# Performance work log

Hardware: AMD Instinct MI355X
Metric: run time of the kernel (lower is better)

Reference implementation:

```python
import jax, jax.numpy as jnp
from jax import lax
import numpy as np

B, T, IN, H, NC = 2048, 512, 1, 128, 8


def setup_inputs() -> dict:
    key = jax.random.key(0)
    ks = jax.random.split(key, 13)
    s = 0.05
    inp = {
        "x": jax.random.normal(ks[0], (B, T, IN), dtype=jnp.float32),
        # layer 0 LSTM params (PyTorch layout: W_ih [4H, in], W_hh [4H, H])
        "W_ih0": jax.random.normal(ks[1], (4 * H, IN), dtype=jnp.float32) * s,
        "W_hh0": jax.random.normal(ks[2], (4 * H, H), dtype=jnp.float32) * s,
        "b_ih0": jax.random.normal(ks[3], (4 * H,), dtype=jnp.float32) * s,
        "b_hh0": jax.random.normal(ks[4], (4 * H,), dtype=jnp.float32) * s,
        # layer 1 LSTM params
        "W_ih1": jax.random.normal(ks[5], (4 * H, H), dtype=jnp.float32) * s,
        "W_hh1": jax.random.normal(ks[6], (4 * H, H), dtype=jnp.float32) * s,
        "b_ih1": jax.random.normal(ks[7], (4 * H,), dtype=jnp.float32) * s,
        "b_hh1": jax.random.normal(ks[8], (4 * H,), dtype=jnp.float32) * s,
        # classifier: Linear(H,64) -> ReLU -> Linear(64,NC)
        "W1": jax.random.normal(ks[9], (64, H), dtype=jnp.float32) * s,
        "b1": jax.random.normal(ks[10], (64,), dtype=jnp.float32) * s,
        "W2": jax.random.normal(ks[11], (NC, 64), dtype=jnp.float32) * s,
        "b2": jax.random.normal(ks[12], (NC,), dtype=jnp.float32) * s,
    }
    return inp


def _lstm_layer(x_seq, W_ih, W_hh, b_ih, b_hh):
    # x_seq: [B, T, in]. PyTorch gate order: i, f, g, o.
    bsz = x_seq.shape[0]
    h_dim = W_hh.shape[1]
    # Precompute input projections for all timesteps (big GEMM outside scan).
    x_proj = jnp.einsum('bti,gi->btg', x_seq, W_ih) + b_ih + b_hh  # [B, T, 4H]

    def step(carry, xp_t):
        h, c = carry
        gates = xp_t + h @ W_hh.T  # [B, 4H]
        i_g, f_g, g_g, o_g = jnp.split(gates, 4, axis=-1)
        i_g = jax.nn.sigmoid(i_g)
        f_g = jax.nn.sigmoid(f_g)
        g_g = jnp.tanh(g_g)
        o_g = jax.nn.sigmoid(o_g)
        c = f_g * c + i_g * g_g
        h = o_g * jnp.tanh(c)
        return (h, c), h

    init = (jnp.zeros((bsz, h_dim), x_seq.dtype), jnp.zeros((bsz, h_dim), x_seq.dtype))
    (_, _), hs = lax.scan(step, init, jnp.swapaxes(x_proj, 0, 1))  # hs: [T, B, H]
    return jnp.swapaxes(hs, 0, 1)  # [B, T, H]


def reference(x, W_ih0, W_hh0, b_ih0, b_hh0, W_ih1, W_hh1, b_ih1, b_hh1, W1, b1, W2, b2):
    h0 = _lstm_layer(x, W_ih0, W_hh0, b_ih0, b_hh0)   # [B, T, H]
    h1 = _lstm_layer(h0, W_ih1, W_hh1, b_ih1, b_hh1)  # [B, T, H] (dropout off in eval)
    last = h1[:, -1, :]                                # [B, H]
    hidden = jax.nn.relu(last @ W1.T + b1)             # [B, 64]
    logits = hidden @ W2.T + b2                        # [B, NC]
    return logits
```

## Files before the change

### kernel.cpp

```cpp
#include <hip/hip_runtime.h>
#include <stdint.h>

typedef float f32x4 __attribute__((ext_vector_type(4)));
typedef short s16x8 __attribute__((ext_vector_type(8)));
typedef short s16x4 __attribute__((ext_vector_type(4)));

#define HDIM 128
#define TLEN 512
#define BT 16

__device__ __forceinline__ unsigned short f2bf(float f) {
    union { float f; uint32_t u; } v; v.f = f;
    uint32_t r = v.u + 0x7FFFu + ((v.u >> 16) & 1u);
    return (unsigned short)(r >> 16);
}
__device__ __forceinline__ float bfhi(uint32_t u){ union{uint32_t u;float f;}v; v.u = u & 0xFFFF0000u; return v.f; }
__device__ __forceinline__ float bflo(uint32_t u){ union{uint32_t u;float f;}v; v.u = u << 16; return v.f; }
__device__ __forceinline__ float bf2f(short s){ union{uint32_t u;float f;}v; v.u = ((uint32_t)(unsigned short)s) << 16; return v.f; }

__device__ __forceinline__ float sigmoidf_(float x){
    float e = __expf(-x);
    return __builtin_amdgcn_rcpf(1.0f + e);
}
__device__ __forceinline__ float tanhf_(float x){
    float e = __expf(2.0f * x);
    return 1.0f - 2.0f * __builtin_amdgcn_rcpf(1.0f + e);
}

__global__ __launch_bounds__(512, 2) void lstm_fused_kernel(
    const float* __restrict__ x,
    const float* __restrict__ Wih0,
    const float* __restrict__ Whh0,
    const float* __restrict__ bih0,
    const float* __restrict__ bhh0,
    const float* __restrict__ Wih1,
    const float* __restrict__ Whh1,
    const float* __restrict__ bih1,
    const float* __restrict__ bhh1,
    const float* __restrict__ W1,
    const float* __restrict__ b1,
    const float* __restrict__ W2,
    const float* __restrict__ b2,
    float* __restrict__ out)
{
    __shared__ __align__(16) short w0lds[65536];
    __shared__ __align__(16) short h0f0[2048], h0f1[2048];
    __shared__ __align__(16) short h1f0[2048], h1f1[2048];
    __shared__ __align__(16) float xlds[64 * 16];

    const int tid = threadIdx.x;
    const int w = tid >> 6;
    const int l = tid & 63;
    const int n = l & 15;
    const int q = l >> 4;
    const int b0 = blockIdx.x * BT;

    s16x8 wi1f[4][4], wh1f[4][4];
    #pragma unroll
    for (int c = 0; c < 4; ++c) {
        #pragma unroll
        for (int tile = 0; tile < 4; ++tile) {
            const int g  = tile * 128 + w * 16 + n;
            const int k0 = c * 32 + q * 8;
            const float* p1 = Wih1 + g * HDIM + k0;
            const float* p2 = Whh1 + g * HDIM + k0;
            s16x8 a, b;
            #pragma unroll
            for (int j = 0; j < 8; ++j) { a[j] = (short)f2bf(p1[j]); b[j] = (short)f2bf(p2[j]); }
            wi1f[c][tile] = a; wh1f[c][tile] = b;
        }
    }

    for (int s2 = tid; s2 < 8192; s2 += 512) {
        const int ll = s2 & 63, tl = (s2 >> 6) & 3, ww = (s2 >> 8) & 7, cc = s2 >> 11;
        const int g  = tl * 128 + ww * 16 + (ll & 15);
        const int k0 = cc * 32 + (ll >> 4) * 8;
        const float* p = Whh0 + g * HDIM + k0;
        s16x8 a;
        #pragma unroll
        for (int j = 0; j < 8; ++j) a[j] = (short)f2bf(p[j]);
        *(s16x8*)&w0lds[s2 * 8] = a;
    }

    const int u0 = w * 16 + q * 4;
    uint32_t b0p[8], b1p[8], wxp[8];
    #pragma unroll
    for (int i = 0; i < 8; ++i) {
        const int tr0 = 2 * i;
        const int tile = tr0 >> 2, r0 = tr0 & 3;
        const int g0 = tile * 128 + u0 + r0;
        const int g1 = g0 + 1;
        b0p[i] = ((uint32_t)f2bf(bih0[g1] + bhh0[g1]) << 16) | f2bf(bih0[g0] + bhh0[g0]);
        b1p[i] = ((uint32_t)f2bf(bih1[g1] + bhh1[g1]) << 16) | f2bf(bih1[g0] + bhh1[g0]);
        wxp[i] = ((uint32_t)f2bf(Wih0[g1]) << 16) | f2bf(Wih0[g0]);
    }

    for (int s2 = tid; s2 < 1024; s2 += 512) {
        ((uint32_t*)h0f1)[s2] = 0u;
        ((uint32_t*)h1f1)[s2] = 0u;
    }

    const int cp  = u0 >> 5;
    const int kbp = (u0 >> 3) & 3;
    const int j0  = u0 & 7;
    const int fragoff = (cp * 64 + (n + 16 * kbp)) * 8 + j0;

    float c0v[4] = {0.f, 0.f, 0.f, 0.f};
    float c1v[4] = {0.f, 0.f, 0.f, 0.f};

    s16x8 hbc[4];
    #pragma unroll
    for (int c = 0; c < 4; ++c) {
        #pragma unroll
        for (int j = 0; j < 8; ++j) hbc[c][j] = 0;
    }

#define REFILL(T) do {                                                        \
    _Pragma("unroll")                                                         \
    for (int i2 = 0; i2 < 2; ++i2) {                                          \
        const int idx = tid + i2 * 512;                                       \
        const int tt = idx & 63, nn = idx >> 6;                               \
        xlds[tt * 16 + nn] = x[(size_t)(b0 + nn) * TLEN + (T) + tt];          \
    }                                                                         \
    __syncthreads();                                                          \
  } while (0)

#define STEP(T, H0W, H1R, H1W) do {                                          \
     \
    const float xv_ = xlds[((T) & 63) * 16 + n];                              \
    f32x4 acc_[4];                                                            \
    _Pragma("unroll")                                                         \
    for (int tile = 0; tile < 4; ++tile) {                                    \
        _Pragma("unroll")                                                     \
        for (int r = 0; r < 4; ++r) {                                         \
            const int tr = tile * 4 + r;                                      \
            const float bb = (tr & 1) ? bfhi(b0p[tr >> 1]) : bflo(b0p[tr >> 1]); \
            const float wv = (tr & 1) ? bfhi(wxp[tr >> 1]) : bflo(wxp[tr >> 1]); \
            acc_[tile][r] = fmaf(wv, xv_, bb);                                \
        }                                                                     \
    }                                                                         \
    _Pragma("unroll")                                                         \
    for (int c = 0; c < 4; ++c) {                                             \
        _Pragma("unroll")                                                     \
        for (int tile = 0; tile < 4; ++tile) {                                \
            const s16x8 a = *(const s16x8*)&w0lds[(((c * 8 + w) * 4 + tile) * 64 + l) * 8]; \
            acc_[tile] = __builtin_amdgcn_mfma_f32_16x16x32_bf16(a, hbc[c], acc_[tile], 0, 0, 0); \
        }                                                                     \
    }                                                                         \
                           \
    {                                                                         \
        s16x4 hw;                                                             \
        _Pragma("unroll")                                                     \
        for (int r = 0; r < 4; ++r) {                                         \
            const float ig = sigmoidf_(acc_[0][r]);                           \
            const float fg = sigmoidf_(acc_[1][r]);                           \
            const float gg = tanhf_(acc_[2][r]);                              \
            const float og = sigmoidf_(acc_[3][r]);                           \
            const float cc = fmaf(fg, c0v[r], ig * gg);                       \
            c0v[r] = cc;                                                      \
            hw[r] = (short)f2bf(og * tanhf_(cc));                             \
        }                                                                     \
        *(s16x4*)&(H0W)[fragoff] = hw;                                        \
    }                                                                         \
    __syncthreads();                                                          \
                 \
    s16x8 hb1_[4];                                                            \
    _Pragma("unroll")                                                         \
    for (int c = 0; c < 4; ++c) {                                             \
        hbc[c]  = *(const s16x8*)&(H0W)[(c * 64 + l) * 8];                    \
        hb1_[c] = *(const s16x8*)&(H1R)[(c * 64 + l) * 8];                    \
    }                                                                         \
    _Pragma("unroll")                                                         \
    for (int tile = 0; tile < 4; ++tile) {                                    \
        _Pragma("unroll")                                                     \
        for (int r = 0; r < 4; ++r) {                                         \
            const int tr = tile * 4 + r;                                      \
            acc_[tile][r] = (tr & 1) ? bfhi(b1p[tr >> 1]) : bflo(b1p[tr >> 1]); \
        }                                                                     \
    }                                                                         \
    _Pragma("unroll")                                                         \
    for (int c = 0; c < 4; ++c) {                                             \
        _Pragma("unroll")                                                     \
        for (int tile = 0; tile < 4; ++tile) {                                \
            acc_[tile] = __builtin_amdgcn_mfma_f32_16x16x32_bf16(wi1f[c][tile], hbc[c], acc_[tile], 0, 0, 0); \
            acc_[tile] = __builtin_amdgcn_mfma_f32_16x16x32_bf16(wh1f[c][tile], hb1_[c], acc_[tile], 0, 0, 0); \
        }                                                                     \
    }                                                                         \
                           \
    {                                                                         \
        s16x4 hw;                                                             \
        _Pragma("unroll")                                                     \
        for (int r = 0; r < 4; ++r) {                                         \
            const float ig = sigmoidf_(acc_[0][r]);                           \
            const float fg = sigmoidf_(acc_[1][r]);                           \
            const float gg = tanhf_(acc_[2][r]);                              \
            const float og = sigmoidf_(acc_[3][r]);                           \
            const float cc = fmaf(fg, c1v[r], ig * gg);                       \
            c1v[r] = cc;                                                      \
            hw[r] = (short)f2bf(og * tanhf_(cc));                             \
        }                                                                     \
        *(s16x4*)&(H1W)[fragoff] = hw;                                        \
    }                                                                         \
  } while (0)

    __syncthreads();

    #pragma unroll 1
    for (int t = 0; t < TLEN; t += 2) {
        if ((t & 63) == 0) REFILL(t);
        STEP(t,     h0f0, h1f1, h1f0);
        STEP(t + 1, h0f1, h1f0, h1f1);
    }

    float* headH = (float*)w0lds;
    float* headL = ((float*)w0lds) + 2048;
    {
        const s16x4 hv = *(const s16x4*)&h1f1[fragoff];
        f32x4 hf;
        #pragma unroll
        for (int r = 0; r < 4; ++r) hf[r] = bf2f(hv[r]);
        __syncthreads();
        *(f32x4*)&headH[n * HDIM + u0] = hf;
    }
    __syncthreads();

    #pragma unroll
    for (int rep = 0; rep < 2; ++rep) {
        const int idx = tid + rep * 512;
        const int nn = idx >> 6, j = idx & 63;
        float s = b1[j];
        const float* wrow = W1 + j * HDIM;
        const float* hrow = headH + nn * HDIM;
        #pragma unroll
        for (int k = 0; k < HDIM; k += 4) {
            const f32x4 hv = *(const f32x4*)&hrow[k];
            const f32x4 wv = *(const f32x4*)&wrow[k];
            s += hv[0]*wv[0] + hv[1]*wv[1] + hv[2]*wv[2] + hv[3]*wv[3];
        }
        headL[nn * 64 + j] = fmaxf(s, 0.0f);
    }
    __syncthreads();

    if (tid < 128) {
        const int nn = tid >> 3, cls = tid & 7;
        float s = b2[cls];
        const float* wrow = W2 + cls * 64;
        const float* hrow = headL + nn * 64;
        #pragma unroll
        for (int k = 0; k < 64; k += 4) {
            const f32x4 hv = *(const f32x4*)&hrow[k];
            const f32x4 wv = *(const f32x4*)&wrow[k];
            s += hv[0]*wv[0] + hv[1]*wv[1] + hv[2]*wv[2] + hv[3]*wv[3];
        }
        out[(size_t)(b0 + nn) * 8 + cls] = s;
    }
}

extern "C" void kernel_launch(void* const* d_in, const int* in_sizes, int n_in,
                              void* d_out, int out_size, void* d_ws, size_t ws_size,
                              hipStream_t stream) {
    const float* x    = (const float*)d_in[0];
    const float* Wih0 = (const float*)d_in[1];
    const float* Whh0 = (const float*)d_in[2];
    const float* bih0 = (const float*)d_in[3];
    const float* bhh0 = (const float*)d_in[4];
    const float* Wih1 = (const float*)d_in[5];
    const float* Whh1 = (const float*)d_in[6];
    const float* bih1 = (const float*)d_in[7];
    const float* bhh1 = (const float*)d_in[8];
    const float* W1   = (const float*)d_in[9];
    const float* b1   = (const float*)d_in[10];
    const float* W2   = (const float*)d_in[11];
    const float* b2   = (const float*)d_in[12];
    float* outp = (float*)d_out;

    lstm_fused_kernel<<<128, 512, 0, stream>>>(
        x, Wih0, Whh0, bih0, bhh0, Wih1, Whh1, bih1, bhh1, W1, b1, W2, b2, outp);
}
```

Before: 1.039 ms.

## Skew LSTM layers by one timestep to merge two barriers into one

Restructures the time loop into a wavefront schedule. Each iteration computes layer-1 step t and layer-0 step t+1 together from the same shared-memory h0 buffer, so each timestep needs one __syncthreads instead of two. The layer-0 step 0 becomes a prologue and the last layer-1 step an epilogue. The x staging through LDS is also dropped in favour of a direct global load per step, which trades the periodic refill barrier for a global memory latency on every step.

```diff
diff --git a/kernel.cpp b/kernel.cpp
--- a/kernel.cpp
+++ b/kernel.cpp
@@ -16,7 +16,6 @@
 }
 __device__ __forceinline__ float bfhi(uint32_t u){ union{uint32_t u;float f;}v; v.u = u & 0xFFFF0000u; return v.f; }
 __device__ __forceinline__ float bflo(uint32_t u){ union{uint32_t u;float f;}v; v.u = u << 16; return v.f; }
-__device__ __forceinline__ float bf2f(short s){ union{uint32_t u;float f;}v; v.u = ((uint32_t)(unsigned short)s) << 16; return v.f; }
 
 __device__ __forceinline__ float sigmoidf_(float x){
     float e = __expf(-x);
@@ -26,6 +25,8 @@
     float e = __expf(2.0f * x);
     return 1.0f - 2.0f * __builtin_amdgcn_rcpf(1.0f + e);
 }
+
+#define UNPK(arr, idx) (((idx) & 1) ? bfhi(arr[(idx) >> 1]) : bflo(arr[(idx) >> 1]))
 
 __global__ __launch_bounds__(512, 2) void lstm_fused_kernel(
     const float* __restrict__ x,
@@ -46,7 +47,6 @@
     __shared__ __align__(16) short w0lds[65536];
     __shared__ __align__(16) short h0f0[2048], h0f1[2048];
     __shared__ __align__(16) short h1f0[2048], h1f1[2048];
-    __shared__ __align__(16) float xlds[64 * 16];
 
     const int tid = threadIdx.x;
     const int w = tid >> 6;
@@ -54,6 +54,7 @@
     const int n = l & 15;
     const int q = l >> 4;
     const int b0 = blockIdx.x * BT;
+    const float* xrow = x + (size_t)(b0 + n) * TLEN;
 
     s16x8 wi1f[4][4], wh1f[4][4];
     #pragma unroll
@@ -95,10 +96,8 @@
         wxp[i] = ((uint32_t)f2bf(Wih0[g1]) << 16) | f2bf(Wih0[g0]);
     }
 
-    for (int s2 = tid; s2 < 1024; s2 += 512) {
-        ((uint32_t*)h0f1)[s2] = 0u;
-        ((uint32_t*)h1f1)[s2] = 0u;
-    }
+    for (int s2 = tid; s2 < 512; s2 += 512) {  }
+    for (int s2 = tid; s2 < 1024; s2 += 512) ((uint32_t*)h1f1)[s2] = 0u;
 
     const int cp  = u0 >> 5;
     const int kbp = (u0 >> 3) & 3;
@@ -107,55 +106,105 @@
 
     float c0v[4] = {0.f, 0.f, 0.f, 0.f};
     float c1v[4] = {0.f, 0.f, 0.f, 0.f};
-
-    s16x8 hbc[4];
-    #pragma unroll
-    for (int c = 0; c < 4; ++c) {
-        #pragma unroll
-        for (int j = 0; j < 8; ++j) hbc[c][j] = 0;
-    }
-
-#define REFILL(T) do {                                                        \
-    _Pragma("unroll")                                                         \
-    for (int i2 = 0; i2 < 2; ++i2) {                                          \
-        const int idx = tid + i2 * 512;                                       \
-        const int tt = idx & 63, nn = idx >> 6;                               \
-        xlds[tt * 16 + nn] = x[(size_t)(b0 + nn) * TLEN + (T) + tt];          \
-    }                                                                         \
-    __syncthreads();                                                          \
-  } while (0)
-
-#define STEP(T, H0W, H1R, H1W) do {                                          \
-     \
-    const float xv_ = xlds[((T) & 63) * 16 + n];                              \
-    f32x4 acc_[4];                                                            \
+    float hfin[4];
+
+    {
+        const float x0v = xrow[0];
+        s16x4 hw;
+        #pragma unroll
+        for (int r = 0; r < 4; ++r) {
+            const float a_i = fmaf(UNPK(wxp, r),      x0v, UNPK(b0p, r));
+            const float a_f = fmaf(UNPK(wxp, 4 + r),  x0v, UNPK(b0p, 4 + r));
+            const float a_g = fmaf(UNPK(wxp, 8 + r),  x0v, UNPK(b0p, 8 + r));
+            const float a_o = fmaf(UNPK(wxp, 12 + r), x0v, UNPK(b0p, 12 + r));
+            const float ig = sigmoidf_(a_i);
+            const float fg = sigmoidf_(a_f); (void)fg;
+            const float gg = tanhf_(a_g);
+            const float og = sigmoidf_(a_o);
+            const float cc = ig * gg;
+            c0v[r] = cc;
+            hw[r] = (short)f2bf(og * tanhf_(cc));
+        }
+        *(s16x4*)&h0f0[fragoff] = hw;
+    }
+    __syncthreads();
+
+#define ITER(T, H0R, H0W, H1R, H1W) do {                                      \
+    const float xnext_ = xrow[(T) + 1];                                       \
+    s16x8 hb0_[4], hb1_[4];                                                   \
+    _Pragma("unroll")                                                         \
+    for (int c = 0; c < 4; ++c) {                                             \
+        hb0_[c] = *(const s16x8*)&(H0R)[(c * 64 + l) * 8];                    \
+        hb1_[c] = *(const s16x8*)&(H1R)[(c * 64 + l) * 8];                    \
+    }                                                                         \
+      \
+    f32x4 acc1_[4];                                                           \
     _Pragma("unroll")                                                         \
     for (int tile = 0; tile < 4; ++tile) {                                    \
-        _Pragma("unroll")                                                     \
-        for (int r = 0; r < 4; ++r) {                                         \
-            const int tr = tile * 4 + r;                                      \
-            const float bb = (tr & 1) ? bfhi(b0p[tr >> 1]) : bflo(b0p[tr >> 1]); \
-            const float wv = (tr & 1) ? bfhi(wxp[tr >> 1]) : bflo(wxp[tr >> 1]); \
-            acc_[tile][r] = fmaf(wv, xv_, bb);                                \
-        }                                                                     \
+        f32x4 cinit;                                                          \
+        _Pragma("unroll")                                                     \
+        for (int r = 0; r < 4; ++r) cinit[r] = UNPK(b1p, tile * 4 + r);       \
+        acc1_[tile] = __builtin_amdgcn_mfma_f32_16x16x32_bf16(wi1f[0][tile], hb0_[0], cinit, 0, 0, 0); \
+    }                                                                         \
+    _Pragma("unroll")                                                         \
+    for (int c = 1; c < 4; ++c) {                                             \
+        _Pragma("unroll")                                                     \
+        for (int tile = 0; tile < 4; ++tile)                                  \
+            acc1_[tile] = __builtin_amdgcn_mfma_f32_16x16x32_bf16(wi1f[c][tile], hb0_[c], acc1_[tile], 0, 0, 0); \
+    }                                                                         \
+    _Pragma("unroll")                                                         \
+    for (int c = 0; c < 4; ++c) {                                             \
+        _Pragma("unroll")                                                     \
+        for (int tile = 0; tile < 4; ++tile)                                  \
+            acc1_[tile] = __builtin_amdgcn_mfma_f32_16x16x32_bf16(wh1f[c][tile], hb1_[c], acc1_[tile], 0, 0, 0); \
+    }                                                                         \
+                 \
+    f32x4 acc0_[4];                                                           \
+    _Pragma("unroll")                                                         \
+    for (int tile = 0; tile < 4; ++tile) {                                    \
+        _Pragma("unroll")                                                     \
+        for (int r = 0; r < 4; ++r) acc0_[tile][r] = 0.0f;                    \
     }                                                                         \
     _Pragma("unroll")                                                         \
     for (int c = 0; c < 4; ++c) {                                             \
         _Pragma("unroll")                                                     \
         for (int tile = 0; tile < 4; ++tile) {                                \
             const s16x8 a = *(const s16x8*)&w0lds[(((c * 8 + w) * 4 + tile) * 64 + l) * 8]; \
-            acc_[tile] = __builtin_amdgcn_mfma_f32_16x16x32_bf16(a, hbc[c], acc_[tile], 0, 0, 0); \
+            acc0_[tile] = __builtin_amdgcn_mfma_f32_16x16x32_bf16(a, hb0_[c], acc0_[tile], 0, 0, 0); \
         }                                                                     \
     }                                                                         \
-                           \
+                                      \
     {                                                                         \
         s16x4 hw;                                                             \
         _Pragma("unroll")                                                     \
         for (int r = 0; r < 4; ++r) {                                         \
-            const float ig = sigmoidf_(acc_[0][r]);                           \
-            const float fg = sigmoidf_(acc_[1][r]);                           \
-            const float gg = tanhf_(acc_[2][r]);                              \
-            const float og = sigmoidf_(acc_[3][r]);                           \
+            const float ig = sigmoidf_(acc1_[0][r]);                          \
+            const float fg = sigmoidf_(acc1_[1][r]);                          \
+            const float gg = tanhf_(acc1_[2][r]);                             \
+            const float og = sigmoidf_(acc1_[3][r]);                          \
+            const float cc = fmaf(fg, c1v[r], ig * gg);                       \
+            c1v[r] = cc;                                                      \
+            hw[r] = (short)f2bf(og * tanhf_(cc));                             \
+        }                                                                     \
+        *(s16x4*)&(H1W)[fragoff] = hw;                                        \
+    }                                                                         \
+           \
+    {                                                                         \
+        s16x4 hw;                                                             \
+        _Pragma("unroll")                                                     \
+        for (int tile = 0; tile < 4; ++tile) {                                \
+            _Pragma("unroll")                                                 \
+            for (int r = 0; r < 4; ++r) {                                     \
+                const int tr = tile * 4 + r;                                  \
+                acc0_[tile][r] += fmaf(UNPK(wxp, tr), xnext_, UNPK(b0p, tr)); \
+            }                                                                 \
+        }                                                                     \
+        _Pragma("unroll")                                                     \
+        for (int r = 0; r < 4; ++r) {                                         \
+            const float ig = sigmoidf_(acc0_[0][r]);                          \
+            const float fg = sigmoidf_(acc0_[1][r]);                          \
+            const float gg = tanhf_(acc0_[2][r]);                             \
+            const float og = sigmoidf_(acc0_[3][r]);                          \
             const float cc = fmaf(fg, c0v[r], ig * gg);                       \
             c0v[r] = cc;                                                      \
             hw[r] = (short)f2bf(og * tanhf_(cc));                             \
@@ -163,63 +212,59 @@
         *(s16x4*)&(H0W)[fragoff] = hw;                                        \
     }                                                                         \
     __syncthreads();                                                          \
-                 \
-    s16x8 hb1_[4];                                                            \
-    _Pragma("unroll")                                                         \
-    for (int c = 0; c < 4; ++c) {                                             \
-        hbc[c]  = *(const s16x8*)&(H0W)[(c * 64 + l) * 8];                    \
-        hb1_[c] = *(const s16x8*)&(H1R)[(c * 64 + l) * 8];                    \
-    }                                                                         \
-    _Pragma("unroll")                                                         \
-    for (int tile = 0; tile < 4; ++tile) {                                    \
-        _Pragma("unroll")                                                     \
-        for (int r = 0; r < 4; ++r) {                                         \
-            const int tr = tile * 4 + r;                                      \
-            acc_[tile][r] = (tr & 1) ? bfhi(b1p[tr >> 1]) : bflo(b1p[tr >> 1]); \
-        }                                                                     \
-    }                                                                         \
-    _Pragma("unroll")                                                         \
-    for (int c = 0; c < 4; ++c) {                                             \
-        _Pragma("unroll")                                                     \
-        for (int tile = 0; tile < 4; ++tile) {                                \
-            acc_[tile] = __builtin_amdgcn_mfma_f32_16x16x32_bf16(wi1f[c][tile], hbc[c], acc_[tile], 0, 0, 0); \
-            acc_[tile] = __builtin_amdgcn_mfma_f32_16x16x32_bf16(wh1f[c][tile], hb1_[c], acc_[tile], 0, 0, 0); \
-        }                                                                     \
-    }                                                                         \
-                           \
-    {                                                                         \
-        s16x4 hw;                                                             \
-        _Pragma("unroll")                                                     \
-        for (int r = 0; r < 4; ++r) {                                         \
-            const float ig = sigmoidf_(acc_[0][r]);                           \
-            const float fg = sigmoidf_(acc_[1][r]);                           \
-            const float gg = tanhf_(acc_[2][r]);                              \
-            const float og = sigmoidf_(acc_[3][r]);                           \
-            const float cc = fmaf(fg, c1v[r], ig * gg);                       \
-            c1v[r] = cc;                                                      \
-            hw[r] = (short)f2bf(og * tanhf_(cc));                             \
-        }                                                                     \
-        *(s16x4*)&(H1W)[fragoff] = hw;                                        \
-    }                                                                         \
-  } while (0)
-
-    __syncthreads();
+} while (0)
 
     #pragma unroll 1
-    for (int t = 0; t < TLEN; t += 2) {
-        if ((t & 63) == 0) REFILL(t);
-        STEP(t,     h0f0, h1f1, h1f0);
-        STEP(t + 1, h0f1, h1f0, h1f1);
+    for (int t = 0; t < 510; t += 2) {
+        ITER(t,     h0f0, h0f1, h1f1, h1f0);
+        ITER(t + 1, h0f1, h0f0, h1f0, h1f1);
+    }
+    ITER(510, h0f0, h0f1, h1f1, h1f0);
+
+    {
+        s16x8 hb0_[4], hb1_[4];
+        #pragma unroll
+        for (int c = 0; c < 4; ++c) {
+            hb0_[c] = *(const s16x8*)&h0f1[(c * 64 + l) * 8];
+            hb1_[c] = *(const s16x8*)&h1f0[(c * 64 + l) * 8];
+        }
+        f32x4 acc1_[4];
+        #pragma unroll
+        for (int tile = 0; tile < 4; ++tile) {
+            f32x4 cinit;
+            #pragma unroll
+            for (int r = 0; r < 4; ++r) cinit[r] = UNPK(b1p, tile * 4 + r);
+            acc1_[tile] = __builtin_amdgcn_mfma_f32_16x16x32_bf16(wi1f[0][tile], hb0_[0], cinit, 0, 0, 0);
+        }
+        #pragma unroll
+        for (int c = 1; c < 4; ++c) {
+            #pragma unroll
+            for (int tile = 0; tile < 4; ++tile)
+                acc1_[tile] = __builtin_amdgcn_mfma_f32_16x16x32_bf16(wi1f[c][tile], hb0_[c], acc1_[tile], 0, 0, 0);
+        }
+        #pragma unroll
+        for (int c = 0; c < 4; ++c) {
+            #pragma unroll
+            for (int tile = 0; tile < 4; ++tile)
+                acc1_[tile] = __builtin_amdgcn_mfma_f32_16x16x32_bf16(wh1f[c][tile], hb1_[c], acc1_[tile], 0, 0, 0);
+        }
+        #pragma unroll
+        for (int r = 0; r < 4; ++r) {
+            const float ig = sigmoidf_(acc1_[0][r]);
+            const float fg = sigmoidf_(acc1_[1][r]);
+            const float gg = tanhf_(acc1_[2][r]);
+            const float og = sigmoidf_(acc1_[3][r]);
+            const float cc = fmaf(fg, c1v[r], ig * gg);
+            hfin[r] = og * tanhf_(cc);
+        }
     }
 
     float* headH = (float*)w0lds;
     float* headL = ((float*)w0lds) + 2048;
     {
-        const s16x4 hv = *(const s16x4*)&h1f1[fragoff];
         f32x4 hf;
         #pragma unroll
-        for (int r = 0; r < 4; ++r) hf[r] = bf2f(hv[r]);
-        __syncthreads();
+        for (int r = 0; r < 4; ++r) hf[r] = hfin[r];
         *(f32x4*)&headH[n * HDIM + u0] = hf;
     }
     __syncthreads();
```

New measurement: 1.007 ms. 1.03x faster.
